# Kernel optimization log

Hardware: AMD Instinct MI355X
Metric: run time of the kernel (lower is better)

The kernel has to match this reference:

```python
import jax, jax.numpy as jnp
import numpy as np


def setup_inputs() -> dict:
    key = jax.random.key(0)
    ks = jax.random.split(key, 5)
    dim = 512
    B, D, H, W = 2, 32, 32, 32
    x = jax.random.normal(ks[0], (B, D, H, W, dim), dtype=jnp.float32)
    # torch nn.Linear-style params stored as [in, out]
    W_qkv = jax.random.normal(ks[1], (dim, 3 * dim), dtype=jnp.float32) * (dim ** -0.5)
    b_qkv = jnp.zeros((3 * dim,), dtype=jnp.float32)
    W_proj = jax.random.normal(ks[2], (dim, dim), dtype=jnp.float32) * (dim ** -0.5)
    b_proj = jnp.zeros((dim,), dtype=jnp.float32)
    return {"x": x, "W_qkv": W_qkv, "b_qkv": b_qkv, "W_proj": W_proj, "b_proj": b_proj}


def reference(x, W_qkv, b_qkv, W_proj, b_proj):
    num_heads = 8
    ws = 4
    B, D, H, W, C = x.shape
    head_dim = C // num_heads
    scale = head_dim ** -0.5
    nd, nh, nw = D // ws, H // ws, W // ws
    num_windows = nd * nh * nw
    T = ws ** 3  # tokens per window

    # window partition: [B, nd, ws, nh, ws, nw, ws, C] -> [B*nwin, T, C]
    xw = x.reshape(B, nd, ws, nh, ws, nw, ws, C)
    xw = xw.transpose(0, 1, 3, 5, 2, 4, 6, 7).reshape(B * num_windows, T, C)

    qkv = xw @ W_qkv + b_qkv  # [N, T, 3C]
    qkv = qkv.reshape(-1, T, 3, num_heads, head_dim).transpose(2, 0, 3, 1, 4)
    q, k, v = qkv[0], qkv[1], qkv[2]  # each [N, heads, T, hd]

    attn = jnp.einsum("nhtd,nhsd->nhts", q, k) * scale
    attn = jnp.clip(attn, -10000.0, 10000.0)
    attn = jax.nn.softmax(attn, axis=-1)
    attn = jnp.nan_to_num(attn, nan=0.0)

    out = jnp.einsum("nhts,nhsd->nhtd", attn, v)  # [N, heads, T, hd]
    out = out.transpose(0, 2, 1, 3).reshape(-1, T, C)
    out = out @ W_proj + b_proj

    # window reverse
    out = out.reshape(B, nd, nh, nw, ws, ws, ws, C)
    out = out.transpose(0, 1, 4, 2, 5, 3, 6, 7).reshape(B, D, H, W, C)
    return out
```

## Files before the change

kernel.cpp:

```cpp
#include <hip/hip_runtime.h>

typedef unsigned int u32;
typedef unsigned short u16;
typedef __attribute__((ext_vector_type(4))) float f32x4;
typedef __attribute__((ext_vector_type(8))) short bf16x8;
typedef __attribute__((ext_vector_type(4))) u32 u32x4;

__device__ __forceinline__ u16 f2bf(float f) {
  u32 u = __builtin_bit_cast(u32, f);
  u = u + 0x7FFFu + ((u >> 16) & 1u);
  return (u16)(u >> 16);
}
__device__ __forceinline__ u32 pack2(float a, float b) {
  return (u32)f2bf(a) | ((u32)f2bf(b) << 16);
}
__device__ __forceinline__ bf16x8 pack8(f32x4 a, f32x4 b) {
  union { u32 w[4]; bf16x8 v; } u;
  u.w[0] = pack2(a[0], a[1]); u.w[1] = pack2(a[2], a[3]);
  u.w[2] = pack2(b[0], b[1]); u.w[3] = pack2(b[2], b[3]);
  return u.v;
}

#define MFMA(a, b, c) __builtin_amdgcn_mfma_f32_16x16x32_bf16((a), (b), (c), 0, 0, 0)

__device__ __forceinline__ bf16x8 lds_frag(const char* buf, int rowBytes, int row, int kByte) {
  return *(const bf16x8*)(buf + row * rowBytes + (kByte ^ ((row & 7) << 4)));
}

__device__ __forceinline__ int tok_global(int blk, int t) {
  int b = blk >> 9, r = blk & 511;
  int wd = r >> 6, wh = (r >> 3) & 7, ww = r & 7;
  int d = wd * 4 + (t >> 4);
  int h = wh * 4 + ((t >> 2) & 3);
  int w = ww * 4 + (t & 3);
  return ((b * 32 + d) * 32 + h) * 32 + w;
}

__global__ void prep_weights(const float* __restrict__ wq, const float* __restrict__ wp,
                             u16* __restrict__ wtq, u16* __restrict__ wtp) {
  int idx = blockIdx.x * 512 + threadIdx.x;
  if (idx < 512 * 1536) {
    int i = idx / 1536, o = idx % 1536;
    int c = i & 31;
    int lane = (c >> 3) * 16 + (o & 15);
    wtq[((size_t)(o >> 4) * 16 + (i >> 5)) * 512 + lane * 8 + (c & 7)] = f2bf(wq[idx]);
  } else {
    int j = idx - 512 * 1536;
    int i = j >> 9, o = j & 511;
    int c = i & 31;
    int lane = (c >> 3) * 16 + (o & 15);
    wtp[((size_t)(o >> 4) * 16 + (i >> 5)) * 512 + lane * 8 + (c & 7)] = f2bf(wp[j]);
  }
}

#define GEMM_PASS_AB(WLANE, SMEMBASE)                                         \
  {                                                                           \
    bf16x8 wfs[3][4], bxs[2][4];                                              \
    _Pragma("unroll") for (int i = 0; i < 4; ++i)                             \
        wfs[0][i] = *(const bf16x8*)((WLANE) + (i * 16 + 0) * 512);           \
    _Pragma("unroll") for (int i = 0; i < 4; ++i)                             \
        wfs[1][i] = *(const bf16x8*)((WLANE) + (i * 16 + 1) * 512);           \
    _Pragma("unroll") for (int j = 0; j < 4; ++j)                             \
        bxs[0][j] = lds_frag((SMEMBASE), 1024, j * 16 + lr, g * 16);          \
    _Pragma("unroll") for (int ks = 0; ks < 16; ++ks) {                       \
      if (ks < 15) {                                                          \
        const int kb1 = (ks + 1) * 64 + g * 16;                               \
        _Pragma("unroll") for (int j = 0; j < 4; ++j)                         \
            bxs[(ks + 1) & 1][j] =                                            \
                lds_frag((SMEMBASE), 1024, j * 16 + lr, kb1);                 \
      }                                                                       \
      if (ks < 14) {                                                          \
        _Pragma("unroll") for (int i = 0; i < 4; ++i)                         \
            wfs[(ks + 2) % 3][i] =                                            \
                *(const bf16x8*)((WLANE) + (i * 16 + ks + 2) * 512);          \
      }                                                                       \
      __builtin_amdgcn_s_setprio(1);                                          \
      _Pragma("unroll") for (int i = 0; i < 4; ++i)                           \
        _Pragma("unroll") for (int j = 0; j < 4; ++j)                         \
            acc[i][j] = MFMA(wfs[ks % 3][i], bxs[ks & 1][j], acc[i][j]);      \
      __builtin_amdgcn_s_setprio(0);                                          \
    }                                                                         \
  }
#define GEMM_PASS_BA(WLANE, SMEMBASE)                                         \
  {                                                                           \
    bf16x8 wfs[3][4], bxs[2][4];                                              \
    _Pragma("unroll") for (int i = 0; i < 4; ++i)                             \
        wfs[0][i] = *(const bf16x8*)((WLANE) + (i * 16 + 0) * 512);           \
    _Pragma("unroll") for (int i = 0; i < 4; ++i)                             \
        wfs[1][i] = *(const bf16x8*)((WLANE) + (i * 16 + 1) * 512);           \
    _Pragma("unroll") for (int j = 0; j < 4; ++j)                             \
        bxs[0][j] = lds_frag((SMEMBASE), 1024, j * 16 + lr, g * 16);          \
    _Pragma("unroll") for (int ks = 0; ks < 16; ++ks) {                       \
      if (ks < 15) {                                                          \
        const int kb1 = (ks + 1) * 64 + g * 16;                               \
        _Pragma("unroll") for (int j = 0; j < 4; ++j)                         \
            bxs[(ks + 1) & 1][j] =                                            \
                lds_frag((SMEMBASE), 1024, j * 16 + lr, kb1);                 \
      }                                                                       \
      if (ks < 14) {                                                          \
        _Pragma("unroll") for (int i = 0; i < 4; ++i)                         \
            wfs[(ks + 2) % 3][i] =                                            \
                *(const bf16x8*)((WLANE) + (i * 16 + ks + 2) * 512);          \
      }                                                                       \
      __builtin_amdgcn_s_setprio(1);                                          \
      _Pragma("unroll") for (int i = 0; i < 4; ++i)                           \
        _Pragma("unroll") for (int j = 0; j < 4; ++j)                         \
            acc[i][j] = MFMA(bxs[ks & 1][i], wfs[ks % 3][j], acc[i][j]);      \
      __builtin_amdgcn_s_setprio(0);                                          \
    }                                                                         \
  }

__global__ __launch_bounds__(512, 2) void fused_win_attn(
    const float* __restrict__ x, const float* __restrict__ bq, const float* __restrict__ bp,
    const u16* __restrict__ wtq, const u16* __restrict__ wtp, float* __restrict__ out) {
  __shared__ char smem[65536];
  const int tid = threadIdx.x;
  const int wv = tid >> 6;
  const int l  = tid & 63;
  const int lr = l & 15;
  const int g  = l >> 4;
  const int blk = blockIdx.x;

  {
    const int st = tid >> 3, seg = tid & 7;
    const float* xs = x + (size_t)tok_global(blk, st) * 512 + seg * 64;
    char* dst = smem + st * 1024;
    const int swz = (st & 7) << 4;
    float4 f[16];
#pragma unroll
    for (int i = 0; i < 16; ++i) f[i] = ((const float4*)xs)[i];
#pragma unroll
    for (int i = 0; i < 8; ++i) {
      const int ic = (i + seg) & 7;
      u32x4 w = {pack2(f[2 * ic].x, f[2 * ic].y),         pack2(f[2 * ic].z, f[2 * ic].w),
                 pack2(f[2 * ic + 1].x, f[2 * ic + 1].y), pack2(f[2 * ic + 1].z, f[2 * ic + 1].w)};
      *(u32x4*)(dst + ((seg * 128 + ic * 16) ^ swz)) = w;
    }
  }
  __syncthreads();

  const u16* wqL = wtq + ((size_t)wv * 4 * 16) * 512 + l * 8;
  const u16* wkL = wqL + (size_t)512 * 512;
  const u16* wvL = wqL + (size_t)1024 * 512;
  const u16* wpL = wtp + ((size_t)wv * 4 * 16) * 512 + l * 8;

  bf16x8 qp[4][2], ka[4][2], pb[4][2], va[4][2];
  f32x4 acc[4][4];

#pragma unroll
  for (int i = 0; i < 4; ++i)
#pragma unroll
    for (int j = 0; j < 4; ++j) acc[i][j] = (f32x4)0.f;
  GEMM_PASS_AB(wqL, smem);
#pragma unroll
  for (int i = 0; i < 4; ++i) {
    const int och = wv * 64 + i * 16 + g * 4;
    f32x4 qb = {bq[och], bq[och + 1], bq[och + 2], bq[och + 3]};
#pragma unroll
    for (int j = 0; j < 4; ++j) acc[i][j] += qb;
  }
#pragma unroll
  for (int j = 0; j < 4; ++j)
#pragma unroll
    for (int kb = 0; kb < 2; ++kb)
      qp[j][kb] = pack8(acc[2 * kb][j], acc[2 * kb + 1][j]);

#pragma unroll
  for (int i = 0; i < 4; ++i)
#pragma unroll
    for (int j = 0; j < 4; ++j) acc[i][j] = (f32x4)0.f;
  GEMM_PASS_AB(wkL, smem);
#pragma unroll
  for (int i = 0; i < 4; ++i) {
    const int och = 512 + wv * 64 + i * 16 + g * 4;
    f32x4 kb = {bq[och], bq[och + 1], bq[och + 2], bq[och + 3]};
#pragma unroll
    for (int j = 0; j < 4; ++j) acc[i][j] += kb;
  }
#pragma unroll
  for (int m = 0; m < 4; ++m)
#pragma unroll
    for (int kb = 0; kb < 2; ++kb)
      ka[m][kb] = pack8(acc[2 * kb][m], acc[2 * kb + 1][m]);

  {
    f32x4 sacc[4][4];
#pragma unroll
    for (int m = 0; m < 4; ++m)
#pragma unroll
      for (int j = 0; j < 4; ++j) {
        f32x4 a = (f32x4)0.f;
        a = MFMA(ka[m][0], qp[j][0], a);
        sacc[m][j] = MFMA(ka[m][1], qp[j][1], a);
      }
#pragma unroll
    for (int m = 0; m < 4; ++m)
#pragma unroll
      for (int j = 0; j < 4; ++j)
#pragma unroll
        for (int r = 0; r < 4; ++r) {
          float v = sacc[m][j][r] * 0.125f;
          sacc[m][j][r] = fminf(fmaxf(v, -10000.f), 10000.f);
        }
    float mx[4], sm[4];
#pragma unroll
    for (int j = 0; j < 4; ++j) {
      float a0 = fmaxf(fmaxf(sacc[0][j][0], sacc[0][j][1]), fmaxf(sacc[0][j][2], sacc[0][j][3]));
      float a1 = fmaxf(fmaxf(sacc[1][j][0], sacc[1][j][1]), fmaxf(sacc[1][j][2], sacc[1][j][3]));
      float a2 = fmaxf(fmaxf(sacc[2][j][0], sacc[2][j][1]), fmaxf(sacc[2][j][2], sacc[2][j][3]));
      float a3 = fmaxf(fmaxf(sacc[3][j][0], sacc[3][j][1]), fmaxf(sacc[3][j][2], sacc[3][j][3]));
      mx[j] = fmaxf(fmaxf(a0, a1), fmaxf(a2, a3));
    }
#pragma unroll
    for (int j = 0; j < 4; ++j) mx[j] = fmaxf(mx[j], __shfl_xor(mx[j], 16));
#pragma unroll
    for (int j = 0; j < 4; ++j) mx[j] = fmaxf(mx[j], __shfl_xor(mx[j], 32));
#pragma unroll
    for (int j = 0; j < 4; ++j) {
      float s0 = 0.f;
#pragma unroll
      for (int m = 0; m < 4; ++m)
#pragma unroll
        for (int r = 0; r < 4; ++r) {
          float p = __expf(sacc[m][j][r] - mx[j]);
          sacc[m][j][r] = p;
          s0 += p;
        }
      sm[j] = s0;
    }
#pragma unroll
    for (int j = 0; j < 4; ++j) sm[j] += __shfl_xor(sm[j], 16);
#pragma unroll
    for (int j = 0; j < 4; ++j) sm[j] += __shfl_xor(sm[j], 32);
#pragma unroll
    for (int j = 0; j < 4; ++j) {
      float inv = 1.f / sm[j];
#pragma unroll
      for (int kb = 0; kb < 2; ++kb)
        pb[j][kb] = pack8(sacc[2 * kb][j] * inv, sacc[2 * kb + 1][j] * inv);
    }
  }

#pragma unroll
  for (int i = 0; i < 4; ++i)
#pragma unroll
    for (int j = 0; j < 4; ++j) acc[i][j] = (f32x4)0.f;
  GEMM_PASS_BA(wvL, smem);
#pragma unroll
  for (int ni = 0; ni < 4; ++ni) {
    float bv = bq[1024 + wv * 64 + ni * 16 + lr];
#pragma unroll
    for (int ti = 0; ti < 4; ++ti) acc[ti][ni] += (f32x4)bv;
#pragma unroll
    for (int kb = 0; kb < 2; ++kb)
      va[ni][kb] = pack8(acc[2 * kb][ni], acc[2 * kb + 1][ni]);
  }

  __syncthreads();

#pragma unroll
  for (int ni = 0; ni < 4; ++ni)
#pragma unroll
    for (int j = 0; j < 4; ++j) {
      f32x4 a = (f32x4)0.f;
      a = MFMA(va[ni][0], pb[j][0], a);
      a = MFMA(va[ni][1], pb[j][1], a);
      int t = j * 16 + lr;
      int cb = (wv * 64 + ni * 16 + g * 4) * 2;
      int swz = (t & 7) << 4;
      *(u32*)(smem + t * 1024 + (cb ^ swz))       = pack2(a[0], a[1]);
      *(u32*)(smem + t * 1024 + ((cb + 4) ^ swz)) = pack2(a[2], a[3]);
    }
  __syncthreads();

#pragma unroll
  for (int i = 0; i < 4; ++i)
#pragma unroll
    for (int j = 0; j < 4; ++j) acc[i][j] = (f32x4)0.f;
  GEMM_PASS_AB(wpL, smem);
#pragma unroll
  for (int mi = 0; mi < 4; ++mi) {
    const int och = wv * 64 + mi * 16 + g * 4;
    f32x4 bb = {bp[och], bp[och + 1], bp[och + 2], bp[och + 3]};
#pragma unroll
    for (int tj = 0; tj < 4; ++tj) acc[mi][tj] += bb;
  }

#pragma unroll
  for (int th = 0; th < 2; ++th) {
    __syncthreads();
#pragma unroll
    for (int mi = 0; mi < 4; ++mi)
#pragma unroll
      for (int jj = 0; jj < 2; ++jj) {
        const int tj = th * 2 + jj;
        const int tl = (tj * 16 + lr) & 31;
        const int ochb = (wv * 64 + mi * 16 + g * 4) * 4;
        *(f32x4*)(smem + tl * 2048 + (ochb ^ ((tl & 7) << 4))) = acc[mi][tj];
      }
    __syncthreads();
#pragma unroll
    for (int it = 0; it < 8; ++it) {
      const int task = it * 8 + wv;
      const int tl = task >> 1;
      const int hf = task & 1;
      const int ochb = hf * 1024 + l * 16;
      f32x4 v = *(const f32x4*)(smem + tl * 2048 + (ochb ^ ((tl & 7) << 4)));
      *(f32x4*)(out + (size_t)tok_global(blk, th * 32 + tl) * 512 + hf * 256 + l * 4) = v;
    }
  }
}

extern "C" void kernel_launch(void* const* d_in, const int* in_sizes, int n_in,
                              void* d_out, int out_size, void* d_ws, size_t ws_size,
                              hipStream_t stream) {
  const float* x  = (const float*)d_in[0];
  const float* wq = (const float*)d_in[1];
  const float* bq = (const float*)d_in[2];
  const float* wp = (const float*)d_in[3];
  const float* bp = (const float*)d_in[4];
  float* out = (float*)d_out;
  u16* wtq = (u16*)d_ws;
  u16* wtp = wtq + 512 * 1536;

  prep_weights<<<2048, 512, 0, stream>>>(wq, wp, wtq, wtp);
  fused_win_attn<<<1024, 512, 0, stream>>>(x, bq, bp, wtq, wtp, out);
}
```

Measured before the change: 222.6 us.

## Stage weight tiles into LDS double buffer via global_load_lds

Replaces per-wave direct global loads of weight fragments (three-deep register prefetch) with block-wide async global_load_lds copies into a double-buffered LDS region. Waves then read their fragments from LDS, with a vmcnt wait and a block barrier after every k-step. The aim is to take weight fetches off the register path and let the DMA-style copy overlap with the MFMAs. In exchange, shared memory per block doubles to 128KB, which likely prevents two blocks per CU. It also adds 16 barriers per GEMM pass and extra LDS traffic, with no cross-wave reuse of the staged weights.

```diff
diff --git a/kernel.cpp b/kernel.cpp
--- a/kernel.cpp
+++ b/kernel.cpp
@@ -53,67 +53,68 @@
   }
 }
 
-#define GEMM_PASS_AB(WLANE, SMEMBASE)                                         \
+__device__ __forceinline__ void stage_w(const char* Wb, char* wbuf, int ks, int tid) {
+#pragma unroll
+  for (int r = 0; r < 4; ++r) {
+    const int flat = r * 8192 + tid * 16;
+    const char* src = Wb + ((size_t)((flat >> 10) * 16 + ks) << 10) + (flat & 1023);
+    __builtin_amdgcn_global_load_lds((const u32*)src, (u32*)(wbuf + flat), 16, 0, 0);
+  }
+}
+
+#define GEMM_PASS_AB(WB)                                                      \
   {                                                                           \
-    bf16x8 wfs[3][4], bxs[2][4];                                              \
-    _Pragma("unroll") for (int i = 0; i < 4; ++i)                             \
-        wfs[0][i] = *(const bf16x8*)((WLANE) + (i * 16 + 0) * 512);           \
-    _Pragma("unroll") for (int i = 0; i < 4; ++i)                             \
-        wfs[1][i] = *(const bf16x8*)((WLANE) + (i * 16 + 1) * 512);           \
-    _Pragma("unroll") for (int j = 0; j < 4; ++j)                             \
-        bxs[0][j] = lds_frag((SMEMBASE), 1024, j * 16 + lr, g * 16);          \
+    stage_w((WB), wb0, 0, tid);                                               \
+    asm volatile("s_waitcnt vmcnt(0)" ::: "memory");                          \
+    __syncthreads();                                                          \
     _Pragma("unroll") for (int ks = 0; ks < 16; ++ks) {                       \
-      if (ks < 15) {                                                          \
-        const int kb1 = (ks + 1) * 64 + g * 16;                               \
-        _Pragma("unroll") for (int j = 0; j < 4; ++j)                         \
-            bxs[(ks + 1) & 1][j] =                                            \
-                lds_frag((SMEMBASE), 1024, j * 16 + lr, kb1);                 \
-      }                                                                       \
-      if (ks < 14) {                                                          \
-        _Pragma("unroll") for (int i = 0; i < 4; ++i)                         \
-            wfs[(ks + 2) % 3][i] =                                            \
-                *(const bf16x8*)((WLANE) + (i * 16 + ks + 2) * 512);          \
-      }                                                                       \
+      if (ks < 15) stage_w((WB), (ks & 1) ? wb0 : wb1, ks + 1, tid);          \
+      char* wb = (ks & 1) ? wb1 : wb0;                                        \
+      bf16x8 bx[4], wf[4];                                                    \
+      const int kByte = ks * 64 + g * 16;                                     \
+      _Pragma("unroll") for (int j = 0; j < 4; ++j)                           \
+          bx[j] = lds_frag(smem, 1024, j * 16 + lr, kByte);                   \
+      _Pragma("unroll") for (int i = 0; i < 4; ++i)                           \
+          wf[i] = *(const bf16x8*)(wb + (wv * 4 + i) * 1024 + l * 16);        \
       __builtin_amdgcn_s_setprio(1);                                          \
       _Pragma("unroll") for (int i = 0; i < 4; ++i)                           \
         _Pragma("unroll") for (int j = 0; j < 4; ++j)                         \
-            acc[i][j] = MFMA(wfs[ks % 3][i], bxs[ks & 1][j], acc[i][j]);      \
+            acc[i][j] = MFMA(wf[i], bx[j], acc[i][j]);                        \
       __builtin_amdgcn_s_setprio(0);                                          \
+      asm volatile("s_waitcnt vmcnt(0)" ::: "memory");                        \
+      __syncthreads();                                                        \
     }                                                                         \
   }
-#define GEMM_PASS_BA(WLANE, SMEMBASE)                                         \
+#define GEMM_PASS_BA(WB)                                                      \
   {                                                                           \
-    bf16x8 wfs[3][4], bxs[2][4];                                              \
-    _Pragma("unroll") for (int i = 0; i < 4; ++i)                             \
-        wfs[0][i] = *(const bf16x8*)((WLANE) + (i * 16 + 0) * 512);           \
-    _Pragma("unroll") for (int i = 0; i < 4; ++i)                             \
-        wfs[1][i] = *(const bf16x8*)((WLANE) + (i * 16 + 1) * 512);           \
-    _Pragma("unroll") for (int j = 0; j < 4; ++j)                             \
-        bxs[0][j] = lds_frag((SMEMBASE), 1024, j * 16 + lr, g * 16);          \
+    stage_w((WB), wb0, 0, tid);                                               \
+    asm volatile("s_waitcnt vmcnt(0)" ::: "memory");                          \
+    __syncthreads();                                                          \
     _Pragma("unroll") for (int ks = 0; ks < 16; ++ks) {                       \
-      if (ks < 15) {                                                          \
-        const int kb1 = (ks + 1) * 64 + g * 16;                               \
-        _Pragma("unroll") for (int j = 0; j < 4; ++j)                         \
-            bxs[(ks + 1) & 1][j] =                                            \
-                lds_frag((SMEMBASE), 1024, j * 16 + lr, kb1);                 \
-      }                                                                       \
-      if (ks < 14) {                                                          \
-        _Pragma("unroll") for (int i = 0; i < 4; ++i)                         \
-            wfs[(ks + 2) % 3][i] =                                            \
-                *(const bf16x8*)((WLANE) + (i * 16 + ks + 2) * 512);          \
-      }                                                                       \
+      if (ks < 15) stage_w((WB), (ks & 1) ? wb0 : wb1, ks + 1, tid);          \
+      char* wb = (ks & 1) ? wb1 : wb0;                                        \
+      bf16x8 bx[4], wf[4];                                                    \
+      const int kByte = ks * 64 + g * 16;                                     \
+      _Pragma("unroll") for (int j = 0; j < 4; ++j)                           \
+          bx[j] = lds_frag(smem, 1024, j * 16 + lr, kByte);                   \
+      _Pragma("unroll") for (int i = 0; i < 4; ++i)                           \
+          wf[i] = *(const bf16x8*)(wb + (wv * 4 + i) * 1024 + l * 16);        \
       __builtin_amdgcn_s_setprio(1);                                          \
       _Pragma("unroll") for (int i = 0; i < 4; ++i)                           \
         _Pragma("unroll") for (int j = 0; j < 4; ++j)                         \
-            acc[i][j] = MFMA(bxs[ks & 1][i], wfs[ks % 3][j], acc[i][j]);      \
+            acc[i][j] = MFMA(bx[i], wf[j], acc[i][j]);                        \
       __builtin_amdgcn_s_setprio(0);                                          \
+      asm volatile("s_waitcnt vmcnt(0)" ::: "memory");                        \
+      __syncthreads();                                                        \
     }                                                                         \
   }
 
 __global__ __launch_bounds__(512, 2) void fused_win_attn(
     const float* __restrict__ x, const float* __restrict__ bq, const float* __restrict__ bp,
     const u16* __restrict__ wtq, const u16* __restrict__ wtp, float* __restrict__ out) {
-  __shared__ char smem[65536];
+  __shared__ char smem[131072];
+  char* wb0 = smem + 65536;
+  char* wb1 = smem + 98304;
   const int tid = threadIdx.x;
   const int wv = tid >> 6;
   const int l  = tid & 63;
@@ -139,10 +140,10 @@
   }
   __syncthreads();
 
-  const u16* wqL = wtq + ((size_t)wv * 4 * 16) * 512 + l * 8;
-  const u16* wkL = wqL + (size_t)512 * 512;
-  const u16* wvL = wqL + (size_t)1024 * 512;
-  const u16* wpL = wtp + ((size_t)wv * 4 * 16) * 512 + l * 8;
+  const char* WQ = (const char*)wtq;
+  const char* WK = WQ + 524288;
+  const char* WV = WQ + 1048576;
+  const char* WP = (const char*)wtp;
 
   bf16x8 qp[4][2], ka[4][2], pb[4][2], va[4][2];
   f32x4 acc[4][4];
@@ -151,7 +152,7 @@
   for (int i = 0; i < 4; ++i)
 #pragma unroll
     for (int j = 0; j < 4; ++j) acc[i][j] = (f32x4)0.f;
-  GEMM_PASS_AB(wqL, smem);
+  GEMM_PASS_AB(WQ);
 #pragma unroll
   for (int i = 0; i < 4; ++i) {
     const int och = wv * 64 + i * 16 + g * 4;
@@ -169,7 +170,7 @@
   for (int i = 0; i < 4; ++i)
 #pragma unroll
     for (int j = 0; j < 4; ++j) acc[i][j] = (f32x4)0.f;
-  GEMM_PASS_AB(wkL, smem);
+  GEMM_PASS_AB(WK);
 #pragma unroll
   for (int i = 0; i < 4; ++i) {
     const int och = 512 + wv * 64 + i * 16 + g * 4;
@@ -245,7 +246,7 @@
   for (int i = 0; i < 4; ++i)
 #pragma unroll
     for (int j = 0; j < 4; ++j) acc[i][j] = (f32x4)0.f;
-  GEMM_PASS_BA(wvL, smem);
+  GEMM_PASS_BA(WV);
 #pragma unroll
   for (int ni = 0; ni < 4; ++ni) {
     float bv = bq[1024 + wv * 64 + ni * 16 + lr];
@@ -277,7 +278,7 @@
   for (int i = 0; i < 4; ++i)
 #pragma unroll
     for (int j = 0; j < 4; ++j) acc[i][j] = (f32x4)0.f;
-  GEMM_PASS_AB(wpL, smem);
+  GEMM_PASS_AB(WP);
 #pragma unroll
   for (int mi = 0; mi < 4; ++mi) {
     const int och = wv * 64 + mi * 16 + g * 4;
```

Result: slower. 276.9 us (+24.4%).
